# Optimization experiments

Measured on AMD Instinct MI355X. Metric: run time of the kernel, lower is better.

Reference implementation:

```python
import jax, jax.numpy as jnp
import numpy as np

B, H, S, D = 1, 16, 4096, 64
NEG = -1.0e9

def setup_inputs() -> dict:
    key = jax.random.key(0)
    kq, kk, kv, km = jax.random.split(key, 4)
    q = jax.random.normal(kq, (B, H, S, D), dtype=jnp.float32)
    k = jax.random.normal(kk, (B, H, S, D), dtype=jnp.float32)
    v = jax.random.normal(kv, (B, H, S, D), dtype=jnp.float32)
    mask = jax.random.randint(km, (1, 1, S, S), 0, 2, dtype=jnp.int32)
    return {"q": q, "k": k, "v": v, "mask": mask}

def reference(q, k, v, mask):
    # BSM=True: q is NOT divided by temperature (matches torch module default)
    attn = jnp.einsum('bhsd,bhtd->bhst', q, k)           # [B,H,S,S]
    attn = jnp.where(mask == 0, NEG, attn)
    attn = jax.nn.softmax(attn, axis=-1)                 # dropout p=0.0 -> identity
    out = jnp.einsum('bhst,bhtd->bhsd', attn, v)         # [B,H,S,D]
    return (out, attn)
```

## Files before the change

### kernel.cpp

```cpp
#include <hip/hip_runtime.h>
#include <cstdint>
#include <cstddef>

typedef unsigned short u16;
typedef unsigned int u32;
typedef __attribute__((ext_vector_type(8))) _Float16 half8;
typedef __attribute__((ext_vector_type(4))) float floatx4;
typedef __attribute__((ext_vector_type(4))) u16 u16x4;
typedef __attribute__((ext_vector_type(8))) u16 u16x8;

#define H_ 16
#define S_ 4096
#define D_ 64
#define BM 64
#define BN 64
#define PAD 68
#define MBW (S_ / 32)

__device__ __forceinline__ u16 f2h(float x) {
  union { _Float16 h; u16 u; } c;
  c.h = (_Float16)x;
  return c.u;
}

__device__ __forceinline__ void st_lds8(u16* p, u16x8 v) {
  union { u16x8 w; u16x4 h[2]; } u; u.w = v;
  *(u16x4*)p = u.h[0];
  *(u16x4*)(p + 4) = u.h[1];
}

__device__ __forceinline__ half8 ld_frag(const u16* p) {
  union { half8 v; u16x4 h[2]; } u;
  u.h[0] = *(const u16x4*)p;
  u.h[1] = *(const u16x4*)(p + 4);
  return u.v;
}

__device__ __forceinline__ void stage_tile(const u16* __restrict__ g, int gstride,
                                           u16* lds, int tid) {
  int r = tid >> 2, c0 = (tid & 3) * 16;
  const u16* src = g + (size_t)r * gstride + c0;
  u16x8 a = *(const u16x8*)(src);
  u16x8 b = *(const u16x8*)(src + 8);
  u16* d = lds + r * PAD + c0;
  st_lds8(d, a);
  st_lds8(d + 8, b);
}

__global__ void prep_qk(const float* __restrict__ q, const float* __restrict__ kk,
                        u16* __restrict__ qb, u16* __restrict__ kb) {
  const size_t N = (size_t)H_ * S_ * D_;
  size_t idx = ((size_t)blockIdx.x * 256 + threadIdx.x) * 8;
  const float* src;
  u16* dst;
  if (idx < N) { src = q + idx; dst = qb + idx; }
  else         { src = kk + (idx - N); dst = kb + (idx - N); }
  float4 f0 = *(const float4*)src;
  float4 f1 = *(const float4*)(src + 4);
  u16x8 o;
  o[0] = f2h(f0.x); o[1] = f2h(f0.y); o[2] = f2h(f0.z); o[3] = f2h(f0.w);
  o[4] = f2h(f1.x); o[5] = f2h(f1.y); o[6] = f2h(f1.z); o[7] = f2h(f1.w);
  *(u16x8*)dst = o;
}

__global__ void prep_vt(const float* __restrict__ v, u16* __restrict__ vt) {
  __shared__ float tile[64][65];
  int h = blockIdx.y, s0 = blockIdx.x * 64;
  int t = threadIdx.x;
  int r = t >> 2, c0 = (t & 3) * 16;
  const float* src = v + ((size_t)(h * S_ + s0 + r)) * D_ + c0;
  #pragma unroll
  for (int i = 0; i < 16; i += 4) {
    float4 f = *(const float4*)(src + i);
    tile[r][c0 + i + 0] = f.x; tile[r][c0 + i + 1] = f.y;
    tile[r][c0 + i + 2] = f.z; tile[r][c0 + i + 3] = f.w;
  }
  __syncthreads();
  u16* dst = vt + ((size_t)(h * D_ + r)) * S_ + s0 + c0;
  u16x8 o0, o1;
  #pragma unroll
  for (int i = 0; i < 8; i++) o0[i] = f2h(tile[c0 + i][r]);
  #pragma unroll
  for (int i = 0; i < 8; i++) o1[i] = f2h(tile[c0 + 8 + i][r]);
  *(u16x8*)dst = o0;
  *(u16x8*)(dst + 8) = o1;
}

__global__ void prep_mask(const int* __restrict__ mask, u32* __restrict__ mb) {
  size_t widx = (size_t)blockIdx.x * 256 + threadIdx.x;
  const int* src = mask + widx * 32;
  u32 bits = 0;
  #pragma unroll
  for (int i = 0; i < 8; i++) {
    int4 m4 = *(const int4*)(src + i * 4);
    bits |= (m4.x != 0 ? 1u : 0u) << (i * 4 + 0);
    bits |= (m4.y != 0 ? 1u : 0u) << (i * 4 + 1);
    bits |= (m4.z != 0 ? 1u : 0u) << (i * 4 + 2);
    bits |= (m4.w != 0 ? 1u : 0u) << (i * 4 + 3);
  }
  mb[widx] = bits;
}

__global__ __launch_bounds__(256, 4)
void attn_fused(const u16* __restrict__ qb, const u16* __restrict__ kb,
                const u16* __restrict__ vt, const u32* __restrict__ mb,
                float* __restrict__ out, float* __restrict__ attn) {
  __shared__ u16 Qs[BM * PAD];
  __shared__ u16 Ks[BN * PAD];
  __shared__ u16 Vts[D_ * PAD];
  __shared__ u16 Ps[BM * PAD];
  __shared__ float Linv[BM];

  const int h = blockIdx.y;
  const int row0 = blockIdx.x * BM;
  const int tid = threadIdx.x;
  const int wave = tid >> 6;
  const int lane = tid & 63;
  const int lrow = lane & 15;
  const int quad = lane >> 4;

  stage_tile(qb + ((size_t)(h * S_ + row0)) * D_, D_, Qs, tid);

  const u16* kbase = kb + (size_t)h * S_ * D_;
  const u16* vbase = vt + (size_t)h * D_ * S_;

  const int arow_off = (wave * 16 + lrow) * PAD;
  const int k0 = quad * 8;
  const int lr0 = wave * 16 + quad * 4;

  float rsum[4] = {0.f, 0.f, 0.f, 0.f};
  for (int j0 = 0; j0 < S_; j0 += BN) {
    __syncthreads();
    stage_tile(kbase + (size_t)j0 * D_, D_, Ks, tid);
    __syncthreads();
    half8 a0 = ld_frag(&Qs[arow_off + k0]);
    half8 a1 = ld_frag(&Qs[arow_off + 32 + k0]);
    u32 mwx[4], mwy[4];
    #pragma unroll
    for (int r = 0; r < 4; r++) {
      const u32* mp = mb + (size_t)(row0 + lr0 + r) * MBW + (j0 >> 5);
      uint2 w = *(const uint2*)mp;
      mwx[r] = w.x; mwy[r] = w.y;
    }
    #pragma unroll
    for (int c = 0; c < 4; c++) {
      half8 b0 = ld_frag(&Ks[(c * 16 + lrow) * PAD + k0]);
      half8 b1 = ld_frag(&Ks[(c * 16 + lrow) * PAD + 32 + k0]);
      floatx4 sc = {0.f, 0.f, 0.f, 0.f};
      sc = __builtin_amdgcn_mfma_f32_16x16x32_f16(a0, b0, sc, 0, 0, 0);
      sc = __builtin_amdgcn_mfma_f32_16x16x32_f16(a1, b1, sc, 0, 0, 0);
      const int sh = (c & 1) * 16 + lrow;
      #pragma unroll
      for (int r = 0; r < 4; r++) {
        u32 w = (c < 2) ? mwx[r] : mwy[r];
        rsum[r] += ((w >> sh) & 1u) ? __expf(sc[r]) : 0.f;
      }
    }
  }
  #pragma unroll
  for (int r = 0; r < 4; r++) {
    float s = rsum[r];
    s += __shfl_xor(s, 1);
    s += __shfl_xor(s, 2);
    s += __shfl_xor(s, 4);
    s += __shfl_xor(s, 8);
    if (lrow == 0) Linv[lr0 + r] = 1.0f / s;
  }
  __syncthreads();
  float linv[4];
  #pragma unroll
  for (int r = 0; r < 4; r++) linv[r] = Linv[lr0 + r];

  floatx4 acc[4];
  #pragma unroll
  for (int c = 0; c < 4; c++) acc[c] = (floatx4){0.f, 0.f, 0.f, 0.f};

  float* attnh = attn + (size_t)h * S_ * S_;

  for (int j0 = 0; j0 < S_; j0 += BN) {
    __syncthreads();
    stage_tile(kbase + (size_t)j0 * D_, D_, Ks, tid);
    stage_tile(vbase + j0, S_, Vts, tid);
    __syncthreads();
    half8 a0 = ld_frag(&Qs[arow_off + k0]);
    half8 a1 = ld_frag(&Qs[arow_off + 32 + k0]);
    u32 mwx[4], mwy[4];
    #pragma unroll
    for (int r = 0; r < 4; r++) {
      const u32* mp = mb + (size_t)(row0 + lr0 + r) * MBW + (j0 >> 5);
      uint2 w = *(const uint2*)mp;
      mwx[r] = w.x; mwy[r] = w.y;
    }
    #pragma unroll
    for (int c = 0; c < 4; c++) {
      half8 b0 = ld_frag(&Ks[(c * 16 + lrow) * PAD + k0]);
      half8 b1 = ld_frag(&Ks[(c * 16 + lrow) * PAD + 32 + k0]);
      floatx4 sc = {0.f, 0.f, 0.f, 0.f};
      sc = __builtin_amdgcn_mfma_f32_16x16x32_f16(a0, b0, sc, 0, 0, 0);
      sc = __builtin_amdgcn_mfma_f32_16x16x32_f16(a1, b1, sc, 0, 0, 0);
      const int sh = (c & 1) * 16 + lrow;
      const int ccol = c * 16 + lrow;
      #pragma unroll
      for (int r = 0; r < 4; r++) {
        u32 w = (c < 2) ? mwx[r] : mwy[r];
        float p = ((w >> sh) & 1u) ? __expf(sc[r]) * linv[r] : 0.f;
        __builtin_nontemporal_store(p, &attnh[(size_t)(row0 + lr0 + r) * S_ + j0 + ccol]);
        Ps[(lr0 + r) * PAD + ccol] = f2h(p);
      }
    }
    __syncthreads();
    half8 p0 = ld_frag(&Ps[arow_off + k0]);
    half8 p1 = ld_frag(&Ps[arow_off + 32 + k0]);
    #pragma unroll
    for (int c = 0; c < 4; c++) {
      half8 v0 = ld_frag(&Vts[(c * 16 + lrow) * PAD + k0]);
      half8 v1 = ld_frag(&Vts[(c * 16 + lrow) * PAD + 32 + k0]);
      acc[c] = __builtin_amdgcn_mfma_f32_16x16x32_f16(p0, v0, acc[c], 0, 0, 0);
      acc[c] = __builtin_amdgcn_mfma_f32_16x16x32_f16(p1, v1, acc[c], 0, 0, 0);
    }
  }

  #pragma unroll
  for (int c = 0; c < 4; c++) {
    #pragma unroll
    for (int r = 0; r < 4; r++) {
      out[((size_t)(h * S_ + row0 + lr0 + r)) * D_ + c * 16 + lrow] = acc[c][r];
    }
  }
}

extern "C" void kernel_launch(void* const* d_in, const int* in_sizes, int n_in,
                              void* d_out, int out_size, void* d_ws, size_t ws_size,
                              hipStream_t stream) {
  const float* q = (const float*)d_in[0];
  const float* k = (const float*)d_in[1];
  const float* v = (const float*)d_in[2];
  const int* mask = (const int*)d_in[3];
  float* out = (float*)d_out;
  float* attn = out + (size_t)H_ * S_ * D_;

  const size_t N = (size_t)H_ * S_ * D_;
  u16* qb = (u16*)d_ws;
  u16* kb = qb + N;
  u16* vt = kb + N;
  u32* mb = (u32*)(vt + N);

  prep_qk<<<dim3((unsigned)(2 * N / (256 * 8))), 256, 0, stream>>>(q, k, qb, kb);
  prep_vt<<<dim3(S_ / 64, H_), 256, 0, stream>>>(v, vt);
  prep_mask<<<dim3((unsigned)(((size_t)S_ * S_ / 32) / 256)), 256, 0, stream>>>(mask, mb);
  attn_fused<<<dim3(S_ / BM, H_), 256, 0, stream>>>(qb, kb, vt, mb, out, attn);
}
```

Baseline: 1.433 ms.

## Swizzle LDS tiles, prefetch K/V via registers, vectorize attn stores

Padded LDS tiles are replaced by unpadded tiles with an XOR swizzle, so fragments can be read with single 16-byte loads. Q fragments now live in registers for the whole kernel instead of being reloaded from LDS each iteration. The next K/V tiles are prefetched into registers while the current tile is in use, overlapping global loads with compute. The attention matrix is written by reading the fp16 P tile back from LDS and storing 8 contiguous floats per lane, replacing scattered scalar stores. The trade-off is that attn is now written from fp16-rounded probabilities, and each thread uses more registers for the prefetch buffers.

```diff
diff --git a/kernel.cpp b/kernel.cpp
--- a/kernel.cpp
+++ b/kernel.cpp
@@ -6,7 +6,6 @@
 typedef unsigned int u32;
 typedef __attribute__((ext_vector_type(8))) _Float16 half8;
 typedef __attribute__((ext_vector_type(4))) float floatx4;
-typedef __attribute__((ext_vector_type(4))) u16 u16x4;
 typedef __attribute__((ext_vector_type(8))) u16 u16x8;
 
 #define H_ 16
@@ -14,7 +13,6 @@
 #define D_ 64
 #define BM 64
 #define BN 64
-#define PAD 68
 #define MBW (S_ / 32)
 
 __device__ __forceinline__ u16 f2h(float x) {
@@ -23,28 +21,31 @@
   return c.u;
 }
 
-__device__ __forceinline__ void st_lds8(u16* p, u16x8 v) {
-  union { u16x8 w; u16x4 h[2]; } u; u.w = v;
-  *(u16x4*)p = u.h[0];
-  *(u16x4*)(p + 4) = u.h[1];
-}
-
-__device__ __forceinline__ half8 ld_frag(const u16* p) {
-  union { half8 v; u16x4 h[2]; } u;
-  u.h[0] = *(const u16x4*)p;
-  u.h[1] = *(const u16x4*)(p + 4);
-  return u.v;
-}
-
-__device__ __forceinline__ void stage_tile(const u16* __restrict__ g, int gstride,
-                                           u16* lds, int tid) {
+__device__ __forceinline__ half8 ld16(const u16* p) {
+  return *(const half8*)p;
+}
+
+__device__ __forceinline__ void glb_pair(const u16* __restrict__ g, int gstride, int tid,
+                                         u16x8& a, u16x8& b) {
   int r = tid >> 2, c0 = (tid & 3) * 16;
   const u16* src = g + (size_t)r * gstride + c0;
-  u16x8 a = *(const u16x8*)(src);
-  u16x8 b = *(const u16x8*)(src + 8);
-  u16* d = lds + r * PAD + c0;
-  st_lds8(d, a);
-  st_lds8(d + 8, b);
+  a = *(const u16x8*)src;
+  b = *(const u16x8*)(src + 8);
+}
+
+__device__ __forceinline__ void stage_regs(u16* lds, int tid, u16x8 a, u16x8 b) {
+  int r = tid >> 2, cb = (tid & 3) * 2, sw = r & 7;
+  u16* base = lds + r * 64;
+  int c0 = (cb ^ sw) << 3;
+  *(u16x8*)(base + c0) = a;
+  *(u16x8*)(base + (c0 ^ 8)) = b;
+}
+
+__device__ __forceinline__ void st_attn8(float* __restrict__ p, half8 v) {
+  floatx4 f0 = { (float)v[0], (float)v[1], (float)v[2], (float)v[3] };
+  floatx4 f1 = { (float)v[4], (float)v[5], (float)v[6], (float)v[7] };
+  __builtin_nontemporal_store(f0, (floatx4*)p);
+  __builtin_nontemporal_store(f1, (floatx4*)(p + 4));
 }
 
 __global__ void prep_qk(const float* __restrict__ q, const float* __restrict__ kk,
@@ -105,10 +106,9 @@
 void attn_fused(const u16* __restrict__ qb, const u16* __restrict__ kb,
                 const u16* __restrict__ vt, const u32* __restrict__ mb,
                 float* __restrict__ out, float* __restrict__ attn) {
-  __shared__ u16 Qs[BM * PAD];
-  __shared__ u16 Ks[BN * PAD];
-  __shared__ u16 Vts[D_ * PAD];
-  __shared__ u16 Ps[BM * PAD];
+  __shared__ __align__(16) u16 Ks[BN * D_];
+  __shared__ __align__(16) u16 Vts[D_ * BN];
+  __shared__ __align__(16) u16 Ps[BM * BN];
   __shared__ float Linv[BM];
 
   const int h = blockIdx.y;
@@ -118,23 +118,29 @@
   const int lane = tid & 63;
   const int lrow = lane & 15;
   const int quad = lane >> 4;
-
-  stage_tile(qb + ((size_t)(h * S_ + row0)) * D_, D_, Qs, tid);
+  const int lr0 = wave * 16 + quad * 4;
+  const int swb = lrow & 7;
+  const int ch0 = (quad ^ swb) << 3;
+  const int ch1 = ((quad + 4) ^ swb) << 3;
+  const int colc = lrow & 7;
+  const int colh = lrow >> 3;
+
+  const u16* qrow = qb + ((size_t)h * S_ + row0 + wave * 16 + lrow) * D_;
+  const half8 a0 = ld16(qrow + quad * 8);
+  const half8 a1 = ld16(qrow + 32 + quad * 8);
 
   const u16* kbase = kb + (size_t)h * S_ * D_;
   const u16* vbase = vt + (size_t)h * D_ * S_;
 
-  const int arow_off = (wave * 16 + lrow) * PAD;
-  const int k0 = quad * 8;
-  const int lr0 = wave * 16 + quad * 4;
-
+  u16x8 kra, krb;
+  glb_pair(kbase, D_, tid, kra, krb);
   float rsum[4] = {0.f, 0.f, 0.f, 0.f};
   for (int j0 = 0; j0 < S_; j0 += BN) {
     __syncthreads();
-    stage_tile(kbase + (size_t)j0 * D_, D_, Ks, tid);
-    __syncthreads();
-    half8 a0 = ld_frag(&Qs[arow_off + k0]);
-    half8 a1 = ld_frag(&Qs[arow_off + 32 + k0]);
+    stage_regs(Ks, tid, kra, krb);
+    int jn = (j0 + BN < S_) ? j0 + BN : 0;
+    glb_pair(kbase + (size_t)jn * D_, D_, tid, kra, krb);
+    __syncthreads();
     u32 mwx[4], mwy[4];
     #pragma unroll
     for (int r = 0; r < 4; r++) {
@@ -144,8 +150,9 @@
     }
     #pragma unroll
     for (int c = 0; c < 4; c++) {
-      half8 b0 = ld_frag(&Ks[(c * 16 + lrow) * PAD + k0]);
-      half8 b1 = ld_frag(&Ks[(c * 16 + lrow) * PAD + 32 + k0]);
+      const u16* krow = Ks + (c * 16 + lrow) * 64;
+      half8 b0 = ld16(krow + ch0);
+      half8 b1 = ld16(krow + ch1);
       floatx4 sc = {0.f, 0.f, 0.f, 0.f};
       sc = __builtin_amdgcn_mfma_f32_16x16x32_f16(a0, b0, sc, 0, 0, 0);
       sc = __builtin_amdgcn_mfma_f32_16x16x32_f16(a1, b1, sc, 0, 0, 0);
@@ -166,6 +173,9 @@
     s += __shfl_xor(s, 8);
     if (lrow == 0) Linv[lr0 + r] = 1.0f / s;
   }
+  u16x8 vra, vrb;
+  glb_pair(kbase, D_, tid, kra, krb);
+  glb_pair(vbase, S_, tid, vra, vrb);
   __syncthreads();
   float linv[4];
   #pragma unroll
@@ -179,11 +189,12 @@
 
   for (int j0 = 0; j0 < S_; j0 += BN) {
     __syncthreads();
-    stage_tile(kbase + (size_t)j0 * D_, D_, Ks, tid);
-    stage_tile(vbase + j0, S_, Vts, tid);
-    __syncthreads();
-    half8 a0 = ld_frag(&Qs[arow_off + k0]);
-    half8 a1 = ld_frag(&Qs[arow_off + 32 + k0]);
+    stage_regs(Ks, tid, kra, krb);
+    stage_regs(Vts, tid, vra, vrb);
+    int jn = (j0 + BN < S_) ? j0 + BN : 0;
+    glb_pair(kbase + (size_t)jn * D_, D_, tid, kra, krb);
+    glb_pair(vbase + jn, S_, tid, vra, vrb);
+    __syncthreads();
     u32 mwx[4], mwy[4];
     #pragma unroll
     for (int r = 0; r < 4; r++) {
@@ -193,28 +204,32 @@
     }
     #pragma unroll
     for (int c = 0; c < 4; c++) {
-      half8 b0 = ld_frag(&Ks[(c * 16 + lrow) * PAD + k0]);
-      half8 b1 = ld_frag(&Ks[(c * 16 + lrow) * PAD + 32 + k0]);
+      const u16* krow = Ks + (c * 16 + lrow) * 64;
+      half8 b0 = ld16(krow + ch0);
+      half8 b1 = ld16(krow + ch1);
       floatx4 sc = {0.f, 0.f, 0.f, 0.f};
       sc = __builtin_amdgcn_mfma_f32_16x16x32_f16(a0, b0, sc, 0, 0, 0);
       sc = __builtin_amdgcn_mfma_f32_16x16x32_f16(a1, b1, sc, 0, 0, 0);
       const int sh = (c & 1) * 16 + lrow;
-      const int ccol = c * 16 + lrow;
       #pragma unroll
       for (int r = 0; r < 4; r++) {
         u32 w = (c < 2) ? mwx[r] : mwy[r];
         float p = ((w >> sh) & 1u) ? __expf(sc[r]) * linv[r] : 0.f;
-        __builtin_nontemporal_store(p, &attnh[(size_t)(row0 + lr0 + r) * S_ + j0 + ccol]);
-        Ps[(lr0 + r) * PAD + ccol] = f2h(p);
+        const int prow = lr0 + r;
+        Ps[prow * 64 + (((2 * c + colh) ^ (prow & 7)) << 3) + colc] = f2h(p);
       }
     }
-    __syncthreads();
-    half8 p0 = ld_frag(&Ps[arow_off + k0]);
-    half8 p1 = ld_frag(&Ps[arow_off + 32 + k0]);
+    const u16* prow = Ps + (wave * 16 + lrow) * 64;
+    half8 p0 = ld16(prow + ch0);
+    half8 p1 = ld16(prow + ch1);
+    float* arow = attnh + (size_t)(row0 + wave * 16 + lrow) * S_ + j0 + quad * 8;
+    st_attn8(arow, p0);
+    st_attn8(arow + 32, p1);
     #pragma unroll
     for (int c = 0; c < 4; c++) {
-      half8 v0 = ld_frag(&Vts[(c * 16 + lrow) * PAD + k0]);
-      half8 v1 = ld_frag(&Vts[(c * 16 + lrow) * PAD + 32 + k0]);
+      const u16* vrow = Vts + (c * 16 + lrow) * 64;
+      half8 v0 = ld16(vrow + ch0);
+      half8 v1 = ld16(vrow + ch1);
       acc[c] = __builtin_amdgcn_mfma_f32_16x16x32_f16(p0, v0, acc[c], 0, 0, 0);
       acc[c] = __builtin_amdgcn_mfma_f32_16x16x32_f16(p1, v1, acc[c], 0, 0, 0);
     }
```

After: 1.447 ms. Within noise of the previous version (+1.0%).
